# Kernel optimization log

Measured on AMD Instinct MI355X. Metric: run time of the kernel, lower is better.

The kernel has to match this reference:

```python
import jax, jax.numpy as jnp
import numpy as np

N = 50000       # nodes
E = 800000      # edges (avg degree 16)
IN_DIM = 128
H_DIM = 96      # conv='SKP' -> h_dim unchanged
OUT_DIM = 64
NUM_LAYERS = 4
HEADS = 2       # conv='SKP' -> num_heads forced to 2


def setup_inputs() -> dict:
    key = jax.random.key(0)
    ks = jax.random.split(key, 9)
    x = jax.random.normal(ks[0], (N, IN_DIM), jnp.float32)
    edge_index = jax.random.randint(ks[1], (2, E), 0, N, dtype=jnp.int32)
    enc_w = jax.random.normal(ks[2], (IN_DIM, H_DIM), jnp.float32) / np.sqrt(IN_DIM)
    enc_b = jnp.zeros((H_DIM,), jnp.float32)
    dec_w = jax.random.normal(ks[3], (H_DIM, OUT_DIM), jnp.float32) / np.sqrt(H_DIM)
    dec_b = jnp.zeros((OUT_DIM,), jnp.float32)
    # per-layer, per-head linear transforms of the SKP conv
    conv_W = jax.random.normal(ks[4], (NUM_LAYERS, HEADS, H_DIM, H_DIM), jnp.float32) / np.sqrt(H_DIM)
    # per-layer, per-head learnable edge weights (SKP takes num_edges at init)
    conv_ew = jax.random.normal(ks[5], (NUM_LAYERS, HEADS, E), jnp.float32) * 0.1
    return {"x": x, "edge_index": edge_index, "enc_w": enc_w, "enc_b": enc_b,
            "dec_w": dec_w, "dec_b": dec_b, "conv_W": conv_W, "conv_ew": conv_ew}


def _skp_conv(h, src, dst, W, ew):
    # h: [N, d], W: [H, d, d], ew: [H, E]
    # X' = sum_h S_h X W_h  (S_h = learned edge-weighted sparse propagation)
    m = jnp.einsum('nd,hde->hne', h, W)          # [H, N, d] per-head transform
    g = m[:, src, :]                              # [H, E, d] gather at source nodes
    comb = jnp.einsum('he,hed->ed', ew, g)        # weight per edge, sum heads -> [E, d]
    return jax.ops.segment_sum(comb, dst, num_segments=N)  # scatter-add to dest


def reference(x, edge_index, enc_w, enc_b, dec_w, dec_b, conv_W, conv_ew):
    src, dst = edge_index[0], edge_index[1]
    h = jax.nn.relu(x @ enc_w + enc_b)
    for l in range(NUM_LAYERS):
        h = _skp_conv(h, src, dst, conv_W[l], conv_ew[l])
        h = jax.nn.relu(h)   # act=True
    return (h @ dec_w + dec_b, h)
```

## Files before the change

### kernel.cpp

```cpp
#include <hip/hip_runtime.h>

constexpr int IND = 128;
constexpr int HD  = 96;
constexpr int OD  = 64;
constexpr int NL  = 4;

struct F3 { float x, y, z; };

__global__ __launch_bounds__(256) void k_hist(const int* __restrict__ dst, int* __restrict__ deg, int E) {
    int e = blockIdx.x * 256 + threadIdx.x;
    if (e < E) atomicAdd(&deg[dst[e]], 1);
}

__global__ __launch_bounds__(256) void k_scan1(const int* __restrict__ deg, int* __restrict__ bsum, int n) {
    int tid = threadIdx.x;
    int base = blockIdx.x * 1024 + tid * 4;
    int s = 0;
    #pragma unroll
    for (int q = 0; q < 4; ++q) { int i = base + q; if (i < n) s += deg[i]; }
    #pragma unroll
    for (int o = 32; o > 0; o >>= 1) s += __shfl_xor(s, o);
    __shared__ int wsum[4];
    int lane = tid & 63, wid = tid >> 6;
    if (lane == 0) wsum[wid] = s;
    __syncthreads();
    if (tid == 0) bsum[blockIdx.x] = wsum[0] + wsum[1] + wsum[2] + wsum[3];
}

__global__ void k_scan2(const int* __restrict__ bsum, int* __restrict__ boff, int nb,
                        int* __restrict__ row_ptr, int n, int E) {
    int l = threadIdx.x;
    int v = (l < nb) ? bsum[l] : 0;
    int incl = v;
    #pragma unroll
    for (int o = 1; o < 64; o <<= 1) { int t = __shfl_up(incl, o); if (l >= o) incl += t; }
    if (l < nb) boff[l] = incl - v;
    if (l == 0) row_ptr[n] = E;
}

__global__ __launch_bounds__(256) void k_scan3(const int* __restrict__ deg, const int* __restrict__ boff,
                                               int* __restrict__ row_ptr, int n) {
    int tid = threadIdx.x;
    int base = blockIdx.x * 1024 + tid * 4;
    int d[4];
    #pragma unroll
    for (int q = 0; q < 4; ++q) { int i = base + q; d[q] = (i < n) ? deg[i] : 0; }
    int tsum = d[0] + d[1] + d[2] + d[3];
    int incl = tsum;
    #pragma unroll
    for (int o = 1; o < 64; o <<= 1) { int t = __shfl_up(incl, o); if ((tid & 63) >= o) incl += t; }
    __shared__ int wsum[4];
    int lane = tid & 63, wid = tid >> 6;
    if (lane == 63) wsum[wid] = incl;
    __syncthreads();
    int woff = 0;
    for (int w = 0; w < wid; ++w) woff += wsum[w];
    int run = boff[blockIdx.x] + woff + (incl - tsum);
    #pragma unroll
    for (int q = 0; q < 4; ++q) {
        int i = base + q;
        if (i < n) { row_ptr[i] = run; run += d[q]; }
    }
}

__global__ __launch_bounds__(256) void k_fill(const int* __restrict__ src, const int* __restrict__ dst,
                                              const int* __restrict__ row_ptr, int* __restrict__ cursor,
                                              int2* __restrict__ sep, int E) {
    int e = blockIdx.x * 256 + threadIdx.x;
    if (e >= E) return;
    int d = dst[e];
    int pos = atomicAdd(&cursor[d], 1);
    sep[row_ptr[d] + pos] = make_int2(src[e], e);
}

__global__ __launch_bounds__(256) void k_perm(const int2* __restrict__ sep,
                                              const float* __restrict__ c0,
                                              const float* __restrict__ c1,
                                              float2* __restrict__ ewq, int E) {
    int i = blockIdx.x * 256 + threadIdx.x;
    if (i >= E) return;
    int e = sep[i].y;
    ewq[i] = make_float2(c0[e], c1[e]);
}

__global__ __launch_bounds__(256) void k_agg(const float* __restrict__ h, const int* __restrict__ row_ptr,
                                             const int2* __restrict__ sep, const float2* __restrict__ ewq,
                                             float* __restrict__ A0, float* __restrict__ A1, int n) {
    int g = blockIdx.x * 8 + (threadIdx.x >> 5);
    int lane = threadIdx.x & 31;
    if (g >= n) return;
    int beg = row_ptr[g], end = row_ptr[g + 1];
    float a0x = 0.f, a0y = 0.f, a0z = 0.f;
    float a1x = 0.f, a1y = 0.f, a1z = 0.f;
    int off = lane * 3;
    int i = beg;
    for (; i + 4 <= end; i += 4) {
        int2 s0 = sep[i], s1 = sep[i + 1], s2 = sep[i + 2], s3 = sep[i + 3];
        float2 w0 = ewq[i], w1 = ewq[i + 1], w2 = ewq[i + 2], w3 = ewq[i + 3];
        F3 v0 = *(const F3*)(h + (size_t)s0.x * HD + off);
        F3 v1 = *(const F3*)(h + (size_t)s1.x * HD + off);
        F3 v2 = *(const F3*)(h + (size_t)s2.x * HD + off);
        F3 v3 = *(const F3*)(h + (size_t)s3.x * HD + off);
        a0x = fmaf(w0.x, v0.x, a0x); a0y = fmaf(w0.x, v0.y, a0y); a0z = fmaf(w0.x, v0.z, a0z);
        a1x = fmaf(w0.y, v0.x, a1x); a1y = fmaf(w0.y, v0.y, a1y); a1z = fmaf(w0.y, v0.z, a1z);
        a0x = fmaf(w1.x, v1.x, a0x); a0y = fmaf(w1.x, v1.y, a0y); a0z = fmaf(w1.x, v1.z, a0z);
        a1x = fmaf(w1.y, v1.x, a1x); a1y = fmaf(w1.y, v1.y, a1y); a1z = fmaf(w1.y, v1.z, a1z);
        a0x = fmaf(w2.x, v2.x, a0x); a0y = fmaf(w2.x, v2.y, a0y); a0z = fmaf(w2.x, v2.z, a0z);
        a1x = fmaf(w2.y, v2.x, a1x); a1y = fmaf(w2.y, v2.y, a1y); a1z = fmaf(w2.y, v2.z, a1z);
        a0x = fmaf(w3.x, v3.x, a0x); a0y = fmaf(w3.x, v3.y, a0y); a0z = fmaf(w3.x, v3.z, a0z);
        a1x = fmaf(w3.y, v3.x, a1x); a1y = fmaf(w3.y, v3.y, a1y); a1z = fmaf(w3.y, v3.z, a1z);
    }
    for (; i < end; ++i) {
        int2 s0 = sep[i];
        float2 w0 = ewq[i];
        F3 v0 = *(const F3*)(h + (size_t)s0.x * HD + off);
        a0x = fmaf(w0.x, v0.x, a0x); a0y = fmaf(w0.x, v0.y, a0y); a0z = fmaf(w0.x, v0.z, a0z);
        a1x = fmaf(w0.y, v0.x, a1x); a1y = fmaf(w0.y, v0.y, a1y); a1z = fmaf(w0.y, v0.z, a1z);
    }
    float* p0 = A0 + (size_t)g * HD + off;
    p0[0] = a0x; p0[1] = a0y; p0[2] = a0z;
    float* p1 = A1 + (size_t)g * HD + off;
    p1[0] = a1x; p1[1] = a1y; p1[2] = a1z;
}

template<int K, int NO, bool DUAL, bool RELU, bool BIAS>
__global__ __launch_bounds__(256) void k_gemm(const float* __restrict__ A0p, const float* __restrict__ A1p,
                                              const float* __restrict__ W0p,
                                              const float* __restrict__ bias,
                                              float* __restrict__ out, int n) {
    constexpr int NC = NO / 32;
    constexpr int F4 = K / 4;
    __shared__ float sA0[64][K];
    __shared__ float sA1[DUAL ? 64 : 1][DUAL ? K : 1];
    int tid = threadIdx.x;
    int brow = blockIdx.x * 64;

    for (int j = tid; j < 64 * F4; j += 256) {
        int r = j / F4, c4 = j % F4;
        int gr = brow + r;
        float4 v = make_float4(0.f, 0.f, 0.f, 0.f);
        if (gr < n) v = *(const float4*)(A0p + (size_t)gr * K + 4 * c4);
        *(float4*)&sA0[r][4 * c4] = v;
        if (DUAL) {
            float4 u = make_float4(0.f, 0.f, 0.f, 0.f);
            if (gr < n) u = *(const float4*)(A1p + (size_t)gr * K + 4 * c4);
            *(float4*)&sA1[r][4 * c4] = u;
        }
    }
    __syncthreads();

    int tx = tid & 31;
    int ty = tid >> 5;
    float acc[8][NC];
    #pragma unroll
    for (int r = 0; r < 8; ++r)
        #pragma unroll
        for (int j = 0; j < NC; ++j) acc[r][j] = 0.f;

    #pragma unroll
    for (int head = 0; head < (DUAL ? 2 : 1); ++head) {
        const float* Wh = W0p + (size_t)head * K * NO;
        #pragma unroll 1
        for (int kb = 0; kb < K; kb += 4) {
            float4 a4[8];
            #pragma unroll
            for (int r = 0; r < 8; ++r)
                a4[r] = head ? *(const float4*)&sA1[8 * ty + r][kb]
                             : *(const float4*)&sA0[8 * ty + r][kb];
            #pragma unroll
            for (int q = 0; q < 4; ++q) {
                float wv[NC];
                #pragma unroll
                for (int j = 0; j < NC; ++j) wv[j] = Wh[(size_t)(kb + q) * NO + NC * tx + j];
                #pragma unroll
                for (int r = 0; r < 8; ++r) {
                    const float* ap = (const float*)&a4[r];
                    float av = ap[q];
                    #pragma unroll
                    for (int j = 0; j < NC; ++j) acc[r][j] = fmaf(av, wv[j], acc[r][j]);
                }
            }
        }
    }
    #pragma unroll
    for (int r = 0; r < 8; ++r) {
        int gr = brow + 8 * ty + r;
        if (gr < n) {
            float* op = out + (size_t)gr * NO + NC * tx;
            #pragma unroll
            for (int j = 0; j < NC; ++j) {
                float v = acc[r][j];
                if (BIAS) v += bias[NC * tx + j];
                if (RELU) v = fmaxf(v, 0.f);
                op[j] = v;
            }
        }
    }
}

extern "C" void kernel_launch(void* const* d_in, const int* in_sizes, int n_in,
                              void* d_out, int out_size, void* d_ws, size_t ws_size,
                              hipStream_t stream) {
    const float* x     = (const float*)d_in[0];
    const int*   ei    = (const int*)  d_in[1];
    const float* enc_w = (const float*)d_in[2];
    const float* enc_b = (const float*)d_in[3];
    const float* dec_w = (const float*)d_in[4];
    const float* dec_b = (const float*)d_in[5];
    const float* convW = (const float*)d_in[6];
    const float* convE = (const float*)d_in[7];

    const int N = in_sizes[0] / IND;
    const int E = in_sizes[1] / 2;
    const int* src = ei;
    const int* dst = ei + E;
    float* fout = (float*)d_out;

    char* wp = (char*)d_ws;
    auto carve = [&](size_t bytes) -> void* {
        void* p = (void*)wp;
        wp += (bytes + 255) & ~(size_t)255;
        return p;
    };
    int*    deg     = (int*)carve(2 * (size_t)N * 4);
    int*    cursor  = deg + N;
    int*    row_ptr = (int*)carve(((size_t)N + 1) * 4);
    int*    bsum    = (int*)carve(64 * 4);
    int*    boff    = (int*)carve(64 * 4);
    int2*   sep     = (int2*)carve((size_t)E * 8);
    float*  P0      = (float*)carve((size_t)N * HD * 4);
    float*  P1      = (float*)carve((size_t)N * HD * 4);
    float*  P2      = (float*)carve((size_t)N * HD * 4);

    float2* ewq = (float2*)fout;

    hipMemsetAsync(deg, 0, 2 * (size_t)N * 4, stream);

    int ebl = (E + 255) / 256;
    int nb  = (N + 1023) / 1024;
    k_hist<<<ebl, 256, 0, stream>>>(dst, deg, E);
    k_scan1<<<nb, 256, 0, stream>>>(deg, bsum, N);
    k_scan2<<<1, 64, 0, stream>>>(bsum, boff, nb, row_ptr, N, E);
    k_scan3<<<nb, 256, 0, stream>>>(deg, boff, row_ptr, N);
    k_fill<<<ebl, 256, 0, stream>>>(src, dst, row_ptr, cursor, sep, E);

    int gbl64 = (N + 63) / 64;
    int gbl8  = (N + 7) / 8;
    float* hfin = fout + (size_t)N * OD;

    k_gemm<IND, HD, false, true, true><<<gbl64, 256, 0, stream>>>(x, nullptr, enc_w, enc_b, P0, N);

    float* hin[NL]  = { P0, P1, P0, P1 };
    float* ha0[NL]  = { P1, P0, P1, P0 };
    float* hout[NL] = { P1, P0, P1, hfin };
    for (int l = 0; l < NL; ++l) {
        const float* c0 = convE + (size_t)(2 * l)     * E;
        const float* c1 = convE + (size_t)(2 * l + 1) * E;
        const float* Wl = convW + (size_t)l * 2 * HD * HD;
        k_perm<<<ebl, 256, 0, stream>>>(sep, c0, c1, ewq, E);
        k_agg<<<gbl8, 256, 0, stream>>>(hin[l], row_ptr, sep, ewq, ha0[l], P2, N);
        k_gemm<HD, HD, true, true, false><<<gbl64, 256, 0, stream>>>(ha0[l], P2, Wl, nullptr, hout[l], N);
    }
    k_gemm<HD, OD, false, false, true><<<gbl64, 256, 0, stream>>>(hfin, nullptr, dec_w, dec_b, fout, N);
}
```

Baseline: 686.4 us.

## Retile dense GEMM to 128-row blocks with swizzled shared memory; batch edge-weight permutes

The dense GEMM now handles 128 rows per block with a 16x16 thread layout, so each thread computes 8 rows by NO/16 columns. Both heads reuse a single shared-memory A tile that is XOR-swizzled to avoid bank conflicts, and W values are read as float2. The goal is more reuse of the W loads and fewer blocks in total, at the cost of higher shared-memory use and register pressure per block, which may lower occupancy. Separately, the edge-weight permutation now runs once per two layers, writing both layers' weights into a buffer twice the size. This halves the number of permute launches and the reads of the sorted edge list.

```diff
diff --git a/kernel.cpp b/kernel.cpp
--- a/kernel.cpp
+++ b/kernel.cpp
@@ -73,14 +73,15 @@
     sep[row_ptr[d] + pos] = make_int2(src[e], e);
 }
 
-__global__ __launch_bounds__(256) void k_perm(const int2* __restrict__ sep,
-                                              const float* __restrict__ c0,
-                                              const float* __restrict__ c1,
-                                              float2* __restrict__ ewq, int E) {
+__global__ __launch_bounds__(256) void k_perm2(const int2* __restrict__ sep,
+                                               const float* __restrict__ cA0, const float* __restrict__ cA1,
+                                               const float* __restrict__ cB0, const float* __restrict__ cB1,
+                                               float2* __restrict__ ewq, int E) {
     int i = blockIdx.x * 256 + threadIdx.x;
     if (i >= E) return;
     int e = sep[i].y;
-    ewq[i] = make_float2(c0[e], c1[e]);
+    ewq[i]     = make_float2(cA0[e], cA1[e]);
+    ewq[E + i] = make_float2(cB0[e], cB1[e]);
 }
 
 __global__ __launch_bounds__(256) void k_agg(const float* __restrict__ h, const int* __restrict__ row_ptr,
@@ -128,29 +129,16 @@
                                               const float* __restrict__ W0p,
                                               const float* __restrict__ bias,
                                               float* __restrict__ out, int n) {
-    constexpr int NC = NO / 32;
-    constexpr int F4 = K / 4;
-    __shared__ float sA0[64][K];
-    __shared__ float sA1[DUAL ? 64 : 1][DUAL ? K : 1];
+    constexpr int BRO = 128;
+    constexpr int KC  = K / 4;
+    constexpr int NC  = NO / 16;
+    __shared__ float sA[BRO * K];
     int tid = threadIdx.x;
-    int brow = blockIdx.x * 64;
-
-    for (int j = tid; j < 64 * F4; j += 256) {
-        int r = j / F4, c4 = j % F4;
-        int gr = brow + r;
-        float4 v = make_float4(0.f, 0.f, 0.f, 0.f);
-        if (gr < n) v = *(const float4*)(A0p + (size_t)gr * K + 4 * c4);
-        *(float4*)&sA0[r][4 * c4] = v;
-        if (DUAL) {
-            float4 u = make_float4(0.f, 0.f, 0.f, 0.f);
-            if (gr < n) u = *(const float4*)(A1p + (size_t)gr * K + 4 * c4);
-            *(float4*)&sA1[r][4 * c4] = u;
-        }
-    }
-    __syncthreads();
-
-    int tx = tid & 31;
-    int ty = tid >> 5;
+    int tx = tid & 15;
+    int ty = tid >> 4;
+    int ty2 = ty & 3;
+    int brow = blockIdx.x * BRO;
+
     float acc[8][NC];
     #pragma unroll
     for (int r = 0; r < 8; ++r)
@@ -159,25 +147,41 @@
 
     #pragma unroll
     for (int head = 0; head < (DUAL ? 2 : 1); ++head) {
+        if (head) __syncthreads();
+        const float* Ah = head ? A1p : A0p;
+        for (int j = tid; j < BRO * KC; j += 256) {
+            int r = j / KC, c4 = j % KC;
+            int gr = brow + r;
+            float4 v = make_float4(0.f, 0.f, 0.f, 0.f);
+            if (gr < n) v = *(const float4*)(Ah + (size_t)gr * K + 4 * c4);
+            int sw = c4 ^ ((r >> 3) & 3);
+            *(float4*)&sA[r * K + 4 * sw] = v;
+        }
+        __syncthreads();
+
         const float* Wh = W0p + (size_t)head * K * NO;
-        #pragma unroll 1
-        for (int kb = 0; kb < K; kb += 4) {
+        #pragma unroll 2
+        for (int kb4 = 0; kb4 < KC; ++kb4) {
             float4 a4[8];
             #pragma unroll
             for (int r = 0; r < 8; ++r)
-                a4[r] = head ? *(const float4*)&sA1[8 * ty + r][kb]
-                             : *(const float4*)&sA0[8 * ty + r][kb];
+                a4[r] = *(const float4*)&sA[(8 * ty + r) * K + 4 * (kb4 ^ ty2)];
             #pragma unroll
             for (int q = 0; q < 4; ++q) {
                 float wv[NC];
+                const float* wrow = Wh + (size_t)(4 * kb4 + q) * NO + NC * tx;
                 #pragma unroll
-                for (int j = 0; j < NC; ++j) wv[j] = Wh[(size_t)(kb + q) * NO + NC * tx + j];
+                for (int j2 = 0; j2 < NC; j2 += 2) {
+                    float2 w2 = *(const float2*)(wrow + j2);
+                    wv[j2] = w2.x; wv[j2 + 1] = w2.y;
+                }
                 #pragma unroll
                 for (int r = 0; r < 8; ++r) {
                     const float* ap = (const float*)&a4[r];
                     float av = ap[q];
                     #pragma unroll
-                    for (int j = 0; j < NC; ++j) acc[r][j] = fmaf(av, wv[j], acc[r][j]);
+                    for (int j2 = 0; j2 < NC; ++j2)
+                        acc[r][j2] = fmaf(av, wv[j2], acc[r][j2]);
                 }
             }
         }
@@ -244,22 +248,26 @@
     k_scan3<<<nb, 256, 0, stream>>>(deg, boff, row_ptr, N);
     k_fill<<<ebl, 256, 0, stream>>>(src, dst, row_ptr, cursor, sep, E);
 
-    int gbl64 = (N + 63) / 64;
-    int gbl8  = (N + 7) / 8;
+    int gblG = (N + 127) / 128;
+    int gbl8 = (N + 7) / 8;
     float* hfin = fout + (size_t)N * OD;
 
-    k_gemm<IND, HD, false, true, true><<<gbl64, 256, 0, stream>>>(x, nullptr, enc_w, enc_b, P0, N);
+    k_gemm<IND, HD, false, true, true><<<gblG, 256, 0, stream>>>(x, nullptr, enc_w, enc_b, P0, N);
 
     float* hin[NL]  = { P0, P1, P0, P1 };
     float* ha0[NL]  = { P1, P0, P1, P0 };
     float* hout[NL] = { P1, P0, P1, hfin };
     for (int l = 0; l < NL; ++l) {
-        const float* c0 = convE + (size_t)(2 * l)     * E;
-        const float* c1 = convE + (size_t)(2 * l + 1) * E;
+        if ((l & 1) == 0) {
+            const float* cA0 = convE + (size_t)(2 * l)     * E;
+            const float* cA1 = convE + (size_t)(2 * l + 1) * E;
+            const float* cB0 = convE + (size_t)(2 * l + 2) * E;
+            const float* cB1 = convE + (size_t)(2 * l + 3) * E;
+            k_perm2<<<ebl, 256, 0, stream>>>(sep, cA0, cA1, cB0, cB1, ewq, E);
+        }
         const float* Wl = convW + (size_t)l * 2 * HD * HD;
-        k_perm<<<ebl, 256, 0, stream>>>(sep, c0, c1, ewq, E);
-        k_agg<<<gbl8, 256, 0, stream>>>(hin[l], row_ptr, sep, ewq, ha0[l], P2, N);
-        k_gemm<HD, HD, true, true, false><<<gbl64, 256, 0, stream>>>(ha0[l], P2, Wl, nullptr, hout[l], N);
-    }
-    k_gemm<HD, OD, false, false, true><<<gbl64, 256, 0, stream>>>(hfin, nullptr, dec_w, dec_b, fout, N);
-}
+        k_agg<<<gbl8, 256, 0, stream>>>(hin[l], row_ptr, sep, ewq + (size_t)(l & 1) * E, ha0[l], P2, N);
+        k_gemm<HD, HD, true, true, false><<<gblG, 256, 0, stream>>>(ha0[l], P2, Wl, nullptr, hout[l], N);
+    }
+    k_gemm<HD, OD, false, false, true><<<gblG, 256, 0, stream>>>(hfin, nullptr, dec_w, dec_b, fout, N);
+}
```

Result: slower. 709.2 us (+3.3%).
